# Optimization experiments

Measured on AMD Instinct MI355X. Metric: run time of the kernel, lower is better.

Reference implementation:

```python
import jax, jax.numpy as jnp
import numpy as np

N = 100000          # nodes
E = 1600000         # edges
IN_DIM = 128
HID = 64
N_CLASSES = 40
N_GAT_LAYERS = 2    # n_layers - 1
ALPHA = 0.2         # LeakyReLU slope
NEG_BIG = -9.0e15


def setup_inputs() -> dict:
    key = jax.random.key(0)
    ks = jax.random.split(key, 8)
    x = jax.random.normal(ks[0], (N, IN_DIM), dtype=jnp.float32)
    edge_index = jax.random.randint(ks[1], (2, E), 0, N, dtype=jnp.int64)
    # parameters (xavier-ish scale)
    emb_w = jax.random.normal(ks[2], (IN_DIM, HID), dtype=jnp.float32) * (1.414 / np.sqrt(IN_DIM + HID))
    emb_b = jnp.zeros((HID,), dtype=jnp.float32)
    Ws = jax.random.normal(ks[3], (N_GAT_LAYERS, HID, HID), dtype=jnp.float32) * (1.414 / np.sqrt(2 * HID))
    attn_a = jax.random.normal(ks[4], (N_GAT_LAYERS, 1, 2 * HID), dtype=jnp.float32) * (1.414 / np.sqrt(1 + 2 * HID))
    out_w = jax.random.normal(ks[5], (HID, N_CLASSES), dtype=jnp.float32) * (1.414 / np.sqrt(HID + N_CLASSES))
    out_b = jnp.zeros((N_CLASSES,), dtype=jnp.float32)
    return {"x": x, "edge_index": edge_index, "emb_w": emb_w, "emb_b": emb_b,
            "Ws": Ws, "attn_a": attn_a, "out_w": out_w, "out_b": out_b}


def _gat_conv(x, edge_src, edge_dst, W, a):
    # x: [N, d_in], W: [d_in, d_out], a: [1, 2*d_out]
    wh = x @ W                                   # [N, d_out]
    d = wh.shape[1]
    a_src = a[0, :d]                             # [d]
    a_dst = a[0, d:]                             # [d]
    # (a * cat(wh[src], wh[dst])).sum(1) == (wh @ a_src)[src] + (wh @ a_dst)[dst]
    s_src = wh @ a_src                           # [N]
    s_dst = wh @ a_dst                           # [N]
    e = jax.nn.leaky_relu(s_src[edge_src] + s_dst[edge_dst], negative_slope=ALPHA)  # [E]
    att = jnp.where(e > 0, e, NEG_BIG)
    att = jax.nn.softmax(att, axis=0)            # GLOBAL softmax over all edges (as in source)
    # scatter-aggregate weighted neighbor features into destination nodes
    msgs = att[:, None] * wh[edge_src]           # [E, d_out]
    h_prime = jax.ops.segment_sum(msgs, edge_dst, num_segments=wh.shape[0])  # [N, d_out]
    return jax.nn.elu(h_prime)                   # concat=True branch


def reference(x, edge_index, emb_w, emb_b, Ws, attn_a, out_w, out_b):
    edge_src = edge_index[0]
    edge_dst = edge_index[1]
    h = x @ emb_w + emb_b                        # emb Linear
    for l in range(N_GAT_LAYERS):
        h = _gat_conv(h, edge_src, edge_dst, Ws[l], attn_a[l])
    h = h @ out_w + out_b                        # out_att Linear
    h = jax.nn.elu(h)
    return jax.nn.log_softmax(h, axis=1)
```

## Files before the change

### kernel.cpp

```cpp
#include <hip/hip_runtime.h>
#include <hip/hip_bf16.h>

#define NODES   100000
#define EDGES   1600000
#define INDIM   128
#define HID     64
#define NCLS    40
#define NEG_BIG_F (-9000000000000000.0f)
#define SENTINEL  (-3.0e38f)

#define BN       512
#define NBUCK    196
#define CHUNK    7168
#define NCHUNK   ((EDGES + CHUNK - 1) / CHUNK)
#define BCAP     8960
#define AGB      3125
#define SMB      128

using bf16x8 = __attribute__((ext_vector_type(8))) short;
using f32x4  = __attribute__((ext_vector_type(4))) float;

static __device__ __forceinline__ float b2f(__hip_bfloat16 h){
    return __bfloat162float(h);
}
static __device__ __forceinline__ float bits2f(unsigned int b){
    union { unsigned int u; float f; } v; v.u = b << 16; return v.f;
}
static __device__ __forceinline__ unsigned short f2b(float f){
    __hip_bfloat16 h = __float2bfloat16(f);
    return *reinterpret_cast<unsigned short*>(&h);
}
static __device__ __forceinline__ float ldin(const void* p, int i, bool f32){
    return f32 ? ((const float*)p)[i] : b2f(((const __hip_bfloat16*)p)[i]);
}
static __device__ __forceinline__ float elu_fast(float x){
    return (x > 0.f) ? x : (__expf(x) - 1.f);
}
static __device__ __forceinline__ unsigned fenc(float f){
    unsigned u = __float_as_uint(f);
    return (u & 0x80000000u) ? ~u : (u | 0x80000000u);
}
static __device__ __forceinline__ float fdec(unsigned k){
    return __uint_as_float((k & 0x80000000u) ? (k & 0x7fffffffu) : ~k);
}
static __device__ __forceinline__ int ld_src(const int* ei, int i, bool i64){
    return i64 ? ei[2*i] : ei[i];
}
static __device__ __forceinline__ int ld_dst(const int* ei, int i, bool i64){
    return i64 ? ei[2*(EDGES + i)] : ei[EDGES + i];
}

__global__ __launch_bounds__(256) void k_detect(const unsigned* __restrict__ xw,
                                                const unsigned* __restrict__ eiw,
                                                int* __restrict__ flags){
    __shared__ int s1[256], s2[256];
    int t = threadIdx.x;
    int c1 = 0, c2 = 0;
    for(int i = t; i < 1024; i += 256){
        unsigned e = (xw[i] >> 23) & 0xffu;
        c1 += (e >= 90u && e <= 160u) ? 1 : 0;
        c2 += (eiw[2*i + 1] == 0u) ? 1 : 0;
    }
    s1[t] = c1; s2[t] = c2; __syncthreads();
    for(int off = 128; off > 0; off >>= 1){
        if(t < off){ s1[t] += s1[t+off]; s2[t] += s2[t+off]; }
        __syncthreads();
    }
    if(t == 0){ flags[0] = (s1[0] > 512) ? 1 : 0; flags[1] = (s2[0] > 512) ? 1 : 0; }
}

__global__ __launch_bounds__(256) void k_bhist(const int* __restrict__ ei,
                                               const int* __restrict__ flags,
                                               int* __restrict__ bdeg){
    __shared__ int sh[NBUCK];
    bool i64 = flags[1] != 0;
    int t = threadIdx.x;
    for(int i = t; i < NBUCK; i += 256) sh[i] = 0;
    __syncthreads();
    int i = blockIdx.x*256 + t;
    int stride = gridDim.x*256;
    for(; i < EDGES; i += stride) atomicAdd(&sh[ld_dst(ei, i, i64) >> 9], 1);
    __syncthreads();
    for(int b = t; b < NBUCK; b += 256) if(sh[b]) atomicAdd(&bdeg[b], sh[b]);
}

__global__ __launch_bounds__(256) void k_bscan(const int* __restrict__ bdeg,
                        int* __restrict__ bstart, int* __restrict__ bcursor){
    __shared__ int sh[256];
    int t = threadIdx.x;
    int v = (t < NBUCK) ? bdeg[t] : 0;
    sh[t] = v; __syncthreads();
    for(int off = 1; off < 256; off <<= 1){
        int x = (t >= off) ? sh[t - off] : 0;
        __syncthreads();
        sh[t] += x;
        __syncthreads();
    }
    int excl = sh[t] - v;
    if(t < NBUCK){ bstart[t] = excl; bcursor[t] = excl; }
    if(t == 255) bstart[NBUCK] = sh[255];
}

__global__ __launch_bounds__(256) void k_bucket_scatter(const int* __restrict__ ei,
    const int* __restrict__ flags, int* __restrict__ bcursor, int2* __restrict__ tmp){
    __shared__ int  sCnt[NBUCK], sScan[NBUCK], sCur[NBUCK], sGofs[NBUCK];
    __shared__ int2 stage[CHUNK];
    bool i64 = flags[1] != 0;
    int t = threadIdx.x;
    int base = blockIdx.x * CHUNK;
    int n = EDGES - base; if(n > CHUNK) n = CHUNK; if(n <= 0) return;

    for(int b = t; b < NBUCK; b += 256) sCnt[b] = 0;
    __syncthreads();
    for(int j = t; j < n; j += 256)
        atomicAdd(&sCnt[ld_dst(ei, base + j, i64) >> 9], 1);
    __syncthreads();
    for(int b = t; b < NBUCK; b += 256) sScan[b] = sCnt[b];
    __syncthreads();
    for(int off = 1; off < NBUCK; off <<= 1){
        int v = 0;
        if(t < NBUCK && t >= off) v = sScan[t - off];
        __syncthreads();
        if(t < NBUCK) sScan[t] += v;
        __syncthreads();
    }
    if(t < NBUCK){
        int excl = sScan[t] - sCnt[t];
        sCur[t]  = excl;
        sGofs[t] = sCnt[t] ? atomicAdd(&bcursor[t], sCnt[t]) : 0;
    }
    __syncthreads();
    for(int j = t; j < n; j += 256){
        int src = ld_src(ei, base + j, i64);
        int dst = ld_dst(ei, base + j, i64);
        int pos = atomicAdd(&sCur[dst >> 9], 1);
        stage[pos] = make_int2(src, dst);
    }
    __syncthreads();
    for(int i = t; i < n; i += 256){
        int2 e = stage[i];
        int  b = e.y >> 9;
        int  excl = sScan[b] - sCnt[b];
        tmp[(size_t)sGofs[b] + (i - excl)] = e;
    }
}

__global__ __launch_bounds__(512) void k_bucket_sort(const int2* __restrict__ tmp,
    const int* __restrict__ bstart, int* __restrict__ col,
    int* __restrict__ rowst){
    __shared__ int  sCnt[BN], sScan[BN], sCur[BN];
    __shared__ int2 stage[BCAP];
    int b = blockIdx.x, t = threadIdx.x;
    int nb0 = b * BN;
    int gbase = bstart[b], gend = bstart[b+1];
    int cnt = gend - gbase;

    if(t < BN) sCnt[t] = 0;
    __syncthreads();
    for(int j = gbase + t; j < gend; j += 512)
        atomicAdd(&sCnt[tmp[j].y - nb0], 1);
    __syncthreads();
    if(t < BN) sScan[t] = sCnt[t];
    __syncthreads();
    for(int off = 1; off < BN; off <<= 1){
        int v = 0;
        if(t < BN && t >= off) v = sScan[t - off];
        __syncthreads();
        if(t < BN) sScan[t] += v;
        __syncthreads();
    }
    if(t < BN) sCur[t] = sScan[t] - sCnt[t];
    if(t < BN && (nb0 + t) < NODES) rowst[nb0 + t] = gbase + (sScan[t] - sCnt[t]);
    if(b == 0 && t == 0) rowst[NODES] = EDGES;
    __syncthreads();
    for(int j = gbase + t; j < gend; j += 512){
        int2 e = tmp[j];
        int pos = atomicAdd(&sCur[e.y - nb0], 1);
        if(pos < BCAP) stage[pos] = e;
        else col[gbase + pos] = e.x;
    }
    __syncthreads();
    int lim = (cnt < BCAP) ? cnt : BCAP;
    for(int i = t; i < lim; i += 512)
        col[gbase + i] = stage[i].x;
}

template<int K, int AMODE, bool WITH_BIAS, bool WITH_SCORES, bool CBF16, int SCALEA>
__global__ __launch_bounds__(256) void k_gemm(
    const void* __restrict__ Aptr,
    const void* __restrict__ Wb,   int woff,
    const void* __restrict__ biasb,
    const void* __restrict__ attnb, int aoff,
    const int*  __restrict__ flags,
    void* __restrict__ Cout,
    float* __restrict__ s_src,
    float* __restrict__ s_dst,
    const float* __restrict__ sdstv,
    const float2* __restrict__ MZg)
{
    __shared__ short As[64][72];
    __shared__ short Bs[64][72];
    const bool wf32 = flags[0] != 0;
    const bool af32 = (AMODE == 2) ? true : ((AMODE == 3) ? false : wf32);
    const int t = threadIdx.x;
    const int block_row = blockIdx.x * 64;
    const int w  = t >> 6;
    const int l  = t & 63;
    const int srow = t >> 2;
    const int sq   = t & 3;
    const int grow_s = block_row + srow;

    float sA = 1.f;
    if constexpr (SCALEA == 1){
        float2 gz = MZg[0];
        float sd = (grow_s < NODES) ? sdstv[grow_s] : 0.f;
        sA = __expf(sd - gz.x) * gz.y;
    }

    f32x4 acc[4] = { {0.f,0.f,0.f,0.f},{0.f,0.f,0.f,0.f},
                     {0.f,0.f,0.f,0.f},{0.f,0.f,0.f,0.f} };

    for(int kb = 0; kb < K; kb += 64){
        {
            unsigned o[16];
            if(af32){
                const float4* av4 = (const float4*)((const float*)Aptr + (size_t)grow_s*K + kb);
                #pragma unroll
                for(int i=0;i<4;i++){
                    float4 u = make_float4(0.f,0.f,0.f,0.f);
                    if(grow_s < NODES) u = av4[sq*4 + i];
                    if constexpr (SCALEA == 1){
                        u.x = elu_fast(u.x*sA); u.y = elu_fast(u.y*sA);
                        u.z = elu_fast(u.z*sA); u.w = elu_fast(u.w*sA);
                    }
                    o[4*i+0]=f2b(u.x); o[4*i+1]=f2b(u.y);
                    o[4*i+2]=f2b(u.z); o[4*i+3]=f2b(u.w);
                }
            } else {
                const uint4* avb = (const uint4*)((const unsigned short*)Aptr + (size_t)grow_s*K + kb);
                #pragma unroll
                for(int i=0;i<2;i++){
                    uint4 u = make_uint4(0,0,0,0);
                    if(grow_s < NODES) u = avb[sq*2 + i];
                    unsigned raw[8] = {u.x&0xffffu, u.x>>16, u.y&0xffffu, u.y>>16,
                                       u.z&0xffffu, u.z>>16, u.w&0xffffu, u.w>>16};
                    if constexpr (SCALEA == 1){
                        #pragma unroll
                        for(int j=0;j<8;j++) raw[j] = f2b(elu_fast(bits2f(raw[j])*sA));
                    }
                    #pragma unroll
                    for(int j=0;j<8;j++) o[8*i+j] = raw[j];
                }
            }
            uint4* dst = (uint4*)&As[srow][sq*16];
            dst[0] = make_uint4(o[0]|(o[1]<<16),  o[2]|(o[3]<<16),
                                o[4]|(o[5]<<16),  o[6]|(o[7]<<16));
            dst[1] = make_uint4(o[8]|(o[9]<<16),  o[10]|(o[11]<<16),
                                o[12]|(o[13]<<16),o[14]|(o[15]<<16));
        }
        if(wf32){
            const float* wv = (const float*)Wb + woff + (size_t)kb*64;
            #pragma unroll
            for(int i=0;i<16;i++){
                int idx = t + 256*i;
                Bs[idx & 63][idx >> 6] = (short)f2b(wv[idx]);
            }
        } else {
            const unsigned short* wv = (const unsigned short*)Wb + woff + (size_t)kb*64;
            #pragma unroll
            for(int i=0;i<16;i++){
                int idx = t + 256*i;
                Bs[idx & 63][idx >> 6] = (short)wv[idx];
            }
        }
        __syncthreads();
        #pragma unroll
        for(int s=0;s<2;s++){
            int k0 = s*32 + 8*(l >> 4);
            bf16x8 a = *(const bf16x8*)&As[16*w + (l & 15)][k0];
            #pragma unroll
            for(int c=0;c<4;c++){
                bf16x8 b = *(const bf16x8*)&Bs[16*c + (l & 15)][k0];
                acc[c] = __builtin_amdgcn_mfma_f32_16x16x32_bf16(a, b, acc[c], 0, 0, 0);
            }
        }
        __syncthreads();
    }

    const int lg4 = (l >> 4) * 4;
    const int lc  = l & 15;
    float bias[4] = {0.f,0.f,0.f,0.f};
    if constexpr (WITH_BIAS){
        #pragma unroll
        for(int c=0;c<4;c++) bias[c] = ldin(biasb, 16*c + lc, wf32);
    }
    #pragma unroll
    for(int r=0;r<4;r++){
        int grow = block_row + 16*w + lg4 + r;
        if(grow < NODES){
            #pragma unroll
            for(int c=0;c<4;c++){
                float vv = acc[c][r] + bias[c];
                if constexpr (CBF16)
                    ((unsigned short*)Cout)[(size_t)grow*64 + 16*c + lc] = f2b(vv);
                else
                    ((float*)Cout)[(size_t)grow*64 + 16*c + lc] = vv;
            }
        }
    }
    if constexpr (WITH_SCORES){
        float as_[4], ad_[4];
        #pragma unroll
        for(int c=0;c<4;c++){
            as_[c] = ldin(attnb, aoff + 16*c + lc, wf32);
            ad_[c] = ldin(attnb, aoff + 64 + 16*c + lc, wf32);
        }
        #pragma unroll
        for(int r=0;r<4;r++){
            float ps = 0.f, pd = 0.f;
            #pragma unroll
            for(int c=0;c<4;c++){
                ps = fmaf(acc[c][r], as_[c], ps);
                pd = fmaf(acc[c][r], ad_[c], pd);
            }
            ps += __shfl_xor(ps, 1, 64); pd += __shfl_xor(pd, 1, 64);
            ps += __shfl_xor(ps, 2, 64); pd += __shfl_xor(pd, 2, 64);
            ps += __shfl_xor(ps, 4, 64); pd += __shfl_xor(pd, 4, 64);
            ps += __shfl_xor(ps, 8, 64); pd += __shfl_xor(pd, 8, 64);
            int grow = block_row + 16*w + lg4 + r;
            if(lc == 0 && grow < NODES){ s_src[grow] = ps; s_dst[grow] = pd; }
        }
    }
}

__global__ __launch_bounds__(256) void k_smax(const float* __restrict__ ssrc,
                                              const float* __restrict__ sdst,
                                              unsigned* __restrict__ smaxk,
                                              unsigned* __restrict__ dmaxk){
    int tid = blockIdx.x*256 + threadIdx.x;
    int stride = gridDim.x*256;
    float m1 = SENTINEL, m2 = SENTINEL;
    for(int i = tid; i < NODES; i += stride){
        m1 = fmaxf(m1, ssrc[i]);
        m2 = fmaxf(m2, sdst[i]);
    }
    #pragma unroll
    for(int off=1; off<64; off<<=1){
        m1 = fmaxf(m1, __shfl_xor(m1, off, 64));
        m2 = fmaxf(m2, __shfl_xor(m2, off, 64));
    }
    __shared__ float sm1[4], sm2[4];
    int w = threadIdx.x >> 6;
    if((threadIdx.x & 63) == 0){ sm1[w] = m1; sm2[w] = m2; }
    __syncthreads();
    if(threadIdx.x == 0){
        for(int i=1;i<4;i++){ m1 = fmaxf(m1, sm1[i]); m2 = fmaxf(m2, sm2[i]); }
        atomicMax(smaxk, fenc(m1));
        atomicMax(dmaxk, fenc(m2));
    }
}

__global__ __launch_bounds__(256) void k_aggregate(const unsigned short* __restrict__ wh16,
    const int* __restrict__ row_start, const int* __restrict__ col,
    const float* __restrict__ ssrc, const float* __restrict__ sdst,
    const unsigned* __restrict__ smaxk, const unsigned* __restrict__ dmaxk,
    unsigned short* __restrict__ U16, float* __restrict__ zpart)
{
    int gw = (blockIdx.x*256 + threadIdx.x) >> 3;
    int l8 = threadIdx.x & 7;
    int sb = (threadIdx.x & 63) & ~7;
    int c8 = l8 * 8;
    int beg = row_start[gw], end = row_start[gw+1];
    float sdn = sdst[gw];
    const float m = fdec(*smaxk) + sdn;
    float zl = 0.f;
    float acc[8] = {0.f,0.f,0.f,0.f,0.f,0.f,0.f,0.f};
    for(int base = beg; base < end; base += 16){
        int idx0 = base + l8;
        int idx1 = base + 8 + l8;
        bool v0 = idx0 < end, v1 = idx1 < end;
        int s0 = v0 ? col[idx0] : 0;
        int s1 = v1 ? col[idx1] : 0;
        float x0 = ssrc[s0] + sdn;
        float x1 = ssrc[s1] + sdn;
        float att0 = (v0 && x0 > 0.f) ? x0 : NEG_BIG_F;
        float att1 = (v1 && x1 > 0.f) ? x1 : NEG_BIG_F;
        float w0 = __expf(att0 - m);
        float w1 = __expf(att1 - m);
        zl += w0 + w1;
        #pragma unroll
        for(int j = 0; j < 8; j++){
            int   s = __shfl(s0, sb + j, 64);
            float a = __shfl(w0, sb + j, 64);
            uint4 u = *(const uint4*)&wh16[(size_t)s*64 + c8];
            acc[0] = fmaf(a, bits2f(u.x & 0xffffu), acc[0]);
            acc[1] = fmaf(a, bits2f(u.x >> 16),     acc[1]);
            acc[2] = fmaf(a, bits2f(u.y & 0xffffu), acc[2]);
            acc[3] = fmaf(a, bits2f(u.y >> 16),     acc[3]);
            acc[4] = fmaf(a, bits2f(u.z & 0xffffu), acc[4]);
            acc[5] = fmaf(a, bits2f(u.z >> 16),     acc[5]);
            acc[6] = fmaf(a, bits2f(u.w & 0xffffu), acc[6]);
            acc[7] = fmaf(a, bits2f(u.w >> 16),     acc[7]);
        }
        #pragma unroll
        for(int j = 0; j < 8; j++){
            int   s = __shfl(s1, sb + j, 64);
            float a = __shfl(w1, sb + j, 64);
            uint4 u = *(const uint4*)&wh16[(size_t)s*64 + c8];
            acc[0] = fmaf(a, bits2f(u.x & 0xffffu), acc[0]);
            acc[1] = fmaf(a, bits2f(u.x >> 16),     acc[1]);
            acc[2] = fmaf(a, bits2f(u.y & 0xffffu), acc[2]);
            acc[3] = fmaf(a, bits2f(u.y >> 16),     acc[3]);
            acc[4] = fmaf(a, bits2f(u.z & 0xffffu), acc[4]);
            acc[5] = fmaf(a, bits2f(u.z >> 16),     acc[5]);
            acc[6] = fmaf(a, bits2f(u.w & 0xffffu), acc[6]);
            acc[7] = fmaf(a, bits2f(u.w >> 16),     acc[7]);
        }
    }
    zl += __shfl_xor(zl, 1, 64);
    zl += __shfl_xor(zl, 2, 64);
    zl += __shfl_xor(zl, 4, 64);
    float zc = (l8 == 0) ? zl * __expf(sdn - fdec(*dmaxk)) : 0.f;
    zc += __shfl_xor(zc, 8, 64);
    zc += __shfl_xor(zc, 16, 64);
    zc += __shfl_xor(zc, 32, 64);
    __shared__ float zsh[4];
    if((threadIdx.x & 63) == 0) zsh[threadIdx.x >> 6] = zc;
    __syncthreads();
    if(threadIdx.x == 0) zpart[blockIdx.x] = zsh[0]+zsh[1]+zsh[2]+zsh[3];
    ushort4 o0 = make_ushort4(f2b(acc[0]), f2b(acc[1]), f2b(acc[2]), f2b(acc[3]));
    ushort4 o1 = make_ushort4(f2b(acc[4]), f2b(acc[5]), f2b(acc[6]), f2b(acc[7]));
    *(ushort4*)&U16[(size_t)gw*64 + c8 + 0] = o0;
    *(ushort4*)&U16[(size_t)gw*64 + c8 + 4] = o1;
}

__global__ __launch_bounds__(256) void k_zfin(const float* __restrict__ zpart,
                                              float2* __restrict__ MZ,
                                              unsigned* __restrict__ smaxk,
                                              unsigned* __restrict__ dmaxk){
    int t = threadIdx.x;
    float z = 0.f;
    for(int i = t; i < AGB; i += 256) z += zpart[i];
    #pragma unroll
    for(int off=1; off<64; off<<=1) z += __shfl_xor(z, off, 64);
    __shared__ float sz[4];
    int w = t >> 6;
    if((t & 63) == 0) sz[w] = z;
    __syncthreads();
    if(t == 0){
        z = sz[0]+sz[1]+sz[2]+sz[3];
        MZ[0] = make_float2(fdec(*dmaxk), 1.0f / z);
        smaxk[0] = 0u;
        dmaxk[0] = 0u;
    }
}

__global__ __launch_bounds__(256) void k_out(const unsigned short* __restrict__ h16,
    const float* __restrict__ sdstv, const float2* __restrict__ MZg,
    const void* __restrict__ Wo, const void* __restrict__ bo,
    const int* __restrict__ flags, float* __restrict__ out)
{
    __shared__ float Ht[64][65];
    __shared__ float Wsh[64][44];
    __shared__ float logits[64][44];
    __shared__ float rlz[64];
    bool f32 = flags[0] != 0;
    int t = threadIdx.x;
    int block_row = blockIdx.x * 64;

    for(int i = t; i < 64*NCLS; i += 256){
        Wsh[i/NCLS][i%NCLS] = ldin(Wo, i, f32);
    }
    {
        int r_load = t >> 2, q = t & 3;
        int grow = block_row + r_load;
        float2 gz = MZg[0];
        float sd = (grow < NODES) ? sdstv[grow] : 0.f;
        float sA = __expf(sd - gz.x) * gz.y;
        const uint4* hv = (const uint4*)h16;
        #pragma unroll
        for(int i = 0; i < 2; i++){
            uint4 u = make_uint4(0,0,0,0);
            if(grow < NODES) u = hv[(size_t)grow*8 + q*2 + i];
            float f[8] = {bits2f(u.x&0xffffu), bits2f(u.x>>16),
                          bits2f(u.y&0xffffu), bits2f(u.y>>16),
                          bits2f(u.z&0xffffu), bits2f(u.z>>16),
                          bits2f(u.w&0xffffu), bits2f(u.w>>16)};
            int k0 = q*16 + i*8;
            #pragma unroll
            for(int j=0;j<8;j++) Ht[k0+j][r_load] = elu_fast(f[j]*sA);
        }
    }
    __syncthreads();

    int cg = t & 15, rg = t >> 4;
    int c0 = cg * 4, r0 = rg * 4;
    if(cg < 10){
        float acc[4][4] = {{0.f,0.f,0.f,0.f},{0.f,0.f,0.f,0.f},{0.f,0.f,0.f,0.f},{0.f,0.f,0.f,0.f}};
        #pragma unroll 8
        for(int k = 0; k < 64; k++){
            float4 a = *(const float4*)&Ht[k][r0];
            float4 w = *(const float4*)&Wsh[k][c0];
            float av4[4] = {a.x,a.y,a.z,a.w};
            float wv4[4] = {w.x,w.y,w.z,w.w};
            #pragma unroll
            for(int i=0;i<4;i++)
                #pragma unroll
                for(int j=0;j<4;j++)
                    acc[i][j] = fmaf(av4[i], wv4[j], acc[i][j]);
        }
        float b[4];
        #pragma unroll
        for(int j=0;j<4;j++) b[j] = ldin(bo, c0+j, f32);
        #pragma unroll
        for(int i=0;i<4;i++)
            #pragma unroll
            for(int j=0;j<4;j++){
                logits[r0+i][c0+j] = elu_fast(acc[i][j] + b[j]);
            }
    }
    __syncthreads();

    {
        int r = t >> 2, qq = t & 3;
        float m = SENTINEL;
        #pragma unroll
        for(int i=0;i<10;i++) m = fmaxf(m, logits[r][qq*10 + i]);
        m = fmaxf(m, __shfl_xor(m, 1, 64));
        m = fmaxf(m, __shfl_xor(m, 2, 64));
        float s = 0.f;
        #pragma unroll
        for(int i=0;i<10;i++) s += __expf(logits[r][qq*10 + i] - m);
        s += __shfl_xor(s, 1, 64);
        s += __shfl_xor(s, 2, 64);
        if(qq == 0) rlz[r] = m + logf(s);
    }
    __syncthreads();

    for(int i = t; i < 64*NCLS; i += 256){
        int rr = i / NCLS, cc = i % NCLS;
        if(block_row + rr < NODES)
            out[(size_t)(block_row)*NCLS + i] = logits[rr][cc] - rlz[rr];
    }
}

extern "C" void kernel_launch(void* const* d_in, const int* in_sizes, int n_in,
                              void* d_out, int out_size, void* d_ws, size_t ws_size,
                              hipStream_t stream)
{
    const void* x      = d_in[0];
    const int*  ei     = (const int*)d_in[1];
    const void* emb_w  = d_in[2];
    const void* emb_b  = d_in[3];
    const void* Ws     = d_in[4];
    const void* attn_a = d_in[5];
    const void* out_w  = d_in[6];
    const void* out_b  = d_in[7];
    float* out = (float*)d_out;

    char* ws = (char*)d_ws;
    size_t off = 0;
    auto alloc = [&](size_t bytes)->char*{
        char* p = ws + off;
        off = (off + bytes + 255) & ~(size_t)255;
        return p;
    };
    int*    flags   = (int*)   alloc(256);
    unsigned short* U16  = (unsigned short*)alloc((size_t)NODES*HID*2);
    unsigned short* h0   = (unsigned short*)alloc((size_t)NODES*HID*2);
    unsigned short* wh16 = (unsigned short*)alloc((size_t)NODES*HID*2);
    float*  ssrc    = (float*) alloc((size_t)NODES*4);
    float*  sdstA   = (float*) alloc((size_t)NODES*4);
    float*  sdstB   = (float*) alloc((size_t)NODES*4);
    int*    rowst   = (int*)   alloc((size_t)(NODES+1)*4);
    int*    col     = (int*)   alloc((size_t)EDGES*4);
    int*    bdeg    = (int*)   alloc(NBUCK*4);
    int*    bstart  = (int*)   alloc((NBUCK+1)*4);
    int*    bcursor = (int*)   alloc(NBUCK*4);
    float*  zpart   = (float*) alloc(AGB*4);
    float2* MZ      = (float2*)alloc(16);
    unsigned* maxk  = (unsigned*)alloc(256);

    int2* tmp = (int2*)U16;

    k_detect<<<1, 256, 0, stream>>>((const unsigned*)x, (const unsigned*)ei, flags);

    hipMemsetAsync(bdeg, 0, NBUCK*4, stream);
    hipMemsetAsync(maxk, 0, 8, stream);
    k_bhist<<<256, 256, 0, stream>>>(ei, flags, bdeg);
    k_bscan<<<1, 256, 0, stream>>>(bdeg, bstart, bcursor);
    k_bucket_scatter<<<NCHUNK, 256, 0, stream>>>(ei, flags, bcursor, tmp);
    k_bucket_sort<<<NBUCK, 512, 0, stream>>>(tmp, bstart, col, rowst);

    k_gemm<INDIM, 0, true, false, true, 0><<<(NODES+63)/64, 256, 0, stream>>>(
        x, emb_w, 0, emb_b, nullptr, 0, flags, h0, nullptr, nullptr, nullptr, nullptr);

    k_gemm<HID, 3, false, true, true, 0><<<(NODES+63)/64, 256, 0, stream>>>(
        h0, Ws, 0, nullptr, attn_a, 0, flags, wh16, ssrc, sdstA, nullptr, nullptr);
    k_smax<<<SMB, 256, 0, stream>>>(ssrc, sdstA, maxk, maxk+1);
    k_aggregate<<<AGB, 256, 0, stream>>>(wh16, rowst, col, ssrc, sdstA, maxk, maxk+1, U16, zpart);
    k_zfin<<<1, 256, 0, stream>>>(zpart, MZ, maxk, maxk+1);

    k_gemm<HID, 3, false, true, true, 1><<<(NODES+63)/64, 256, 0, stream>>>(
        U16, Ws, HID*HID, nullptr, attn_a, 2*HID, flags, wh16, ssrc, sdstB, sdstA, MZ);
    k_smax<<<SMB, 256, 0, stream>>>(ssrc, sdstB, maxk, maxk+1);
    k_aggregate<<<AGB, 256, 0, stream>>>(wh16, rowst, col, ssrc, sdstB, maxk, maxk+1, U16, zpart);
    k_zfin<<<1, 256, 0, stream>>>(zpart, MZ, maxk, maxk+1);

    k_out<<<(NODES+63)/64, 256, 0, stream>>>(U16, sdstB, MZ, out_w, out_b, flags, out);
}
```

Before: 307.5 us.

## Pack bucketed edges into 32-bit words, use MFMA for output linear, fold memset

Bucket-sort edges are now packed as src plus local dst offset in a single int instead of int2, with bucket id kept in a byte array. This halves the temporary edge traffic and shared-memory staging in the scatter and sort kernels. The output classification GEMM now uses bf16 MFMA instead of scalar FMA, which adds bf16 rounding of activations and weights. One memset is removed by clearing the max keys inside the scan kernel.

```diff
diff --git a/kernel.cpp b/kernel.cpp
--- a/kernel.cpp
+++ b/kernel.cpp
@@ -85,7 +85,8 @@
 }
 
 __global__ __launch_bounds__(256) void k_bscan(const int* __restrict__ bdeg,
-                        int* __restrict__ bstart, int* __restrict__ bcursor){
+                        int* __restrict__ bstart, int* __restrict__ bcursor,
+                        unsigned* __restrict__ maxk){
     __shared__ int sh[256];
     int t = threadIdx.x;
     int v = (t < NBUCK) ? bdeg[t] : 0;
@@ -99,12 +100,14 @@
     int excl = sh[t] - v;
     if(t < NBUCK){ bstart[t] = excl; bcursor[t] = excl; }
     if(t == 255) bstart[NBUCK] = sh[255];
+    if(t == 0){ maxk[0] = 0u; maxk[1] = 0u; }
 }
 
 __global__ __launch_bounds__(256) void k_bucket_scatter(const int* __restrict__ ei,
-    const int* __restrict__ flags, int* __restrict__ bcursor, int2* __restrict__ tmp){
+    const int* __restrict__ flags, int* __restrict__ bcursor, int* __restrict__ tmp){
     __shared__ int  sCnt[NBUCK], sScan[NBUCK], sCur[NBUCK], sGofs[NBUCK];
-    __shared__ int2 stage[CHUNK];
+    __shared__ int  stage[CHUNK];
+    __shared__ unsigned char bId[CHUNK];
     bool i64 = flags[1] != 0;
     int t = threadIdx.x;
     int base = blockIdx.x * CHUNK;
@@ -133,23 +136,25 @@
     for(int j = t; j < n; j += 256){
         int src = ld_src(ei, base + j, i64);
         int dst = ld_dst(ei, base + j, i64);
-        int pos = atomicAdd(&sCur[dst >> 9], 1);
-        stage[pos] = make_int2(src, dst);
+        int b   = dst >> 9;
+        int pos = atomicAdd(&sCur[b], 1);
+        stage[pos] = src | ((dst & 511) << 17);
+        bId[pos]   = (unsigned char)b;
     }
     __syncthreads();
     for(int i = t; i < n; i += 256){
-        int2 e = stage[i];
-        int  b = e.y >> 9;
-        int  excl = sScan[b] - sCnt[b];
+        int e = stage[i];
+        int b = bId[i];
+        int excl = sScan[b] - sCnt[b];
         tmp[(size_t)sGofs[b] + (i - excl)] = e;
     }
 }
 
-__global__ __launch_bounds__(512) void k_bucket_sort(const int2* __restrict__ tmp,
+__global__ __launch_bounds__(512) void k_bucket_sort(const int* __restrict__ tmp,
     const int* __restrict__ bstart, int* __restrict__ col,
     int* __restrict__ rowst){
-    __shared__ int  sCnt[BN], sScan[BN], sCur[BN];
-    __shared__ int2 stage[BCAP];
+    __shared__ int sCnt[BN], sScan[BN], sCur[BN];
+    __shared__ int stage[BCAP];
     int b = blockIdx.x, t = threadIdx.x;
     int nb0 = b * BN;
     int gbase = bstart[b], gend = bstart[b+1];
@@ -158,7 +163,7 @@
     if(t < BN) sCnt[t] = 0;
     __syncthreads();
     for(int j = gbase + t; j < gend; j += 512)
-        atomicAdd(&sCnt[tmp[j].y - nb0], 1);
+        atomicAdd(&sCnt[tmp[j] >> 17], 1);
     __syncthreads();
     if(t < BN) sScan[t] = sCnt[t];
     __syncthreads();
@@ -174,15 +179,15 @@
     if(b == 0 && t == 0) rowst[NODES] = EDGES;
     __syncthreads();
     for(int j = gbase + t; j < gend; j += 512){
-        int2 e = tmp[j];
-        int pos = atomicAdd(&sCur[e.y - nb0], 1);
+        int e = tmp[j];
+        int pos = atomicAdd(&sCur[e >> 17], 1);
         if(pos < BCAP) stage[pos] = e;
-        else col[gbase + pos] = e.x;
+        else col[gbase + pos] = e & 0x1FFFF;
     }
     __syncthreads();
     int lim = (cnt < BCAP) ? cnt : BCAP;
     for(int i = t; i < lim; i += 512)
-        col[gbase + i] = stage[i].x;
+        col[gbase + i] = stage[i] & 0x1FFFF;
 }
 
 template<int K, int AMODE, bool WITH_BIAS, bool WITH_SCORES, bool CBF16, int SCALEA>
@@ -460,64 +465,70 @@
     const void* __restrict__ Wo, const void* __restrict__ bo,
     const int* __restrict__ flags, float* __restrict__ out)
 {
-    __shared__ float Ht[64][65];
-    __shared__ float Wsh[64][44];
+    __shared__ short As[64][72];
+    __shared__ short Bs[48][72];
     __shared__ float logits[64][44];
     __shared__ float rlz[64];
     bool f32 = flags[0] != 0;
     int t = threadIdx.x;
     int block_row = blockIdx.x * 64;
-
+    const int w = t >> 6, l = t & 63;
+    const int srow = t >> 2, sq = t & 3;
+    const int grow_s = block_row + srow;
+
+    {
+        float2 gz = MZg[0];
+        float sd = (grow_s < NODES) ? sdstv[grow_s] : 0.f;
+        float sA = __expf(sd - gz.x) * gz.y;
+        unsigned o[16];
+        const uint4* avb = (const uint4*)(h16 + (size_t)grow_s*64);
+        #pragma unroll
+        for(int i=0;i<2;i++){
+            uint4 u = make_uint4(0,0,0,0);
+            if(grow_s < NODES) u = avb[sq*2 + i];
+            unsigned raw[8] = {u.x&0xffffu, u.x>>16, u.y&0xffffu, u.y>>16,
+                               u.z&0xffffu, u.z>>16, u.w&0xffffu, u.w>>16};
+            #pragma unroll
+            for(int j=0;j<8;j++) o[8*i+j] = f2b(elu_fast(bits2f(raw[j])*sA));
+        }
+        uint4* dst = (uint4*)&As[srow][sq*16];
+        dst[0] = make_uint4(o[0]|(o[1]<<16),  o[2]|(o[3]<<16),
+                            o[4]|(o[5]<<16),  o[6]|(o[7]<<16));
+        dst[1] = make_uint4(o[8]|(o[9]<<16),  o[10]|(o[11]<<16),
+                            o[12]|(o[13]<<16),o[14]|(o[15]<<16));
+    }
+    for(int i = t; i < 8*64; i += 256) Bs[40 + (i>>6)][i & 63] = 0;
     for(int i = t; i < 64*NCLS; i += 256){
-        Wsh[i/NCLS][i%NCLS] = ldin(Wo, i, f32);
+        int k = i / NCLS, c = i % NCLS;
+        Bs[c][k] = (short)(f32 ? f2b(((const float*)Wo)[i])
+                               : ((const unsigned short*)Wo)[i]);
+    }
+    __syncthreads();
+
+    f32x4 acc[3] = { {0.f,0.f,0.f,0.f},{0.f,0.f,0.f,0.f},{0.f,0.f,0.f,0.f} };
+    #pragma unroll
+    for(int s=0;s<2;s++){
+        int k0 = s*32 + 8*(l >> 4);
+        bf16x8 a = *(const bf16x8*)&As[16*w + (l & 15)][k0];
+        #pragma unroll
+        for(int c=0;c<3;c++){
+            bf16x8 b = *(const bf16x8*)&Bs[16*c + (l & 15)][k0];
+            acc[c] = __builtin_amdgcn_mfma_f32_16x16x32_bf16(a, b, acc[c], 0, 0, 0);
+        }
     }
     {
-        int r_load = t >> 2, q = t & 3;
-        int grow = block_row + r_load;
-        float2 gz = MZg[0];
-        float sd = (grow < NODES) ? sdstv[grow] : 0.f;
-        float sA = __expf(sd - gz.x) * gz.y;
-        const uint4* hv = (const uint4*)h16;
-        #pragma unroll
-        for(int i = 0; i < 2; i++){
-            uint4 u = make_uint4(0,0,0,0);
-            if(grow < NODES) u = hv[(size_t)grow*8 + q*2 + i];
-            float f[8] = {bits2f(u.x&0xffffu), bits2f(u.x>>16),
-                          bits2f(u.y&0xffffu), bits2f(u.y>>16),
-                          bits2f(u.z&0xffffu), bits2f(u.z>>16),
-                          bits2f(u.w&0xffffu), bits2f(u.w>>16)};
-            int k0 = q*16 + i*8;
-            #pragma unroll
-            for(int j=0;j<8;j++) Ht[k0+j][r_load] = elu_fast(f[j]*sA);
-        }
-    }
-    __syncthreads();
-
-    int cg = t & 15, rg = t >> 4;
-    int c0 = cg * 4, r0 = rg * 4;
-    if(cg < 10){
-        float acc[4][4] = {{0.f,0.f,0.f,0.f},{0.f,0.f,0.f,0.f},{0.f,0.f,0.f,0.f},{0.f,0.f,0.f,0.f}};
-        #pragma unroll 8
-        for(int k = 0; k < 64; k++){
-            float4 a = *(const float4*)&Ht[k][r0];
-            float4 w = *(const float4*)&Wsh[k][c0];
-            float av4[4] = {a.x,a.y,a.z,a.w};
-            float wv4[4] = {w.x,w.y,w.z,w.w};
-            #pragma unroll
-            for(int i=0;i<4;i++)
+        const int lg4 = (l >> 4) * 4;
+        const int lc  = l & 15;
+        #pragma unroll
+        for(int c=0;c<3;c++){
+            int colv = 16*c + lc;
+            if(colv < NCLS){
+                float bia = ldin(bo, colv, f32);
                 #pragma unroll
-                for(int j=0;j<4;j++)
-                    acc[i][j] = fmaf(av4[i], wv4[j], acc[i][j]);
-        }
-        float b[4];
-        #pragma unroll
-        for(int j=0;j<4;j++) b[j] = ldin(bo, c0+j, f32);
-        #pragma unroll
-        for(int i=0;i<4;i++)
-            #pragma unroll
-            for(int j=0;j<4;j++){
-                logits[r0+i][c0+j] = elu_fast(acc[i][j] + b[j]);
+                for(int r=0;r<4;r++)
+                    logits[16*w + lg4 + r][colv] = elu_fast(acc[c][r] + bia);
             }
+        }
     }
     __syncthreads();
 
@@ -581,14 +592,13 @@
     float2* MZ      = (float2*)alloc(16);
     unsigned* maxk  = (unsigned*)alloc(256);
 
-    int2* tmp = (int2*)U16;
+    int* tmp = (int*)U16;
 
     k_detect<<<1, 256, 0, stream>>>((const unsigned*)x, (const unsigned*)ei, flags);
 
     hipMemsetAsync(bdeg, 0, NBUCK*4, stream);
-    hipMemsetAsync(maxk, 0, 8, stream);
     k_bhist<<<256, 256, 0, stream>>>(ei, flags, bdeg);
-    k_bscan<<<1, 256, 0, stream>>>(bdeg, bstart, bcursor);
+    k_bscan<<<1, 256, 0, stream>>>(bdeg, bstart, bcursor, maxk);
     k_bucket_scatter<<<NCHUNK, 256, 0, stream>>>(ei, flags, bcursor, tmp);
     k_bucket_sort<<<NBUCK, 512, 0, stream>>>(tmp, bstart, col, rowst);
 
```

Result: faster. 293.7 us (-4.5%).
